# Kernel optimization log

Measured on AMD Instinct MI355X. Metric: run time of the kernel, lower is better.

Reference implementation:

```python
import jax, jax.numpy as jnp
import numpy as np

N = 50000      # nodes
E = 800000     # edges
D = 128        # d_model
H = 8          # heads
DH = D // H    # head dim
FF = 512       # dim_ff
NB = 32        # degree buckets
EPS = 1e-5


def _ln(x, g, b):
    mu = jnp.mean(x, axis=-1, keepdims=True)
    var = jnp.mean((x - mu) ** 2, axis=-1, keepdims=True)
    return (x - mu) * jax.lax.rsqrt(var + EPS) * g + b


def setup_inputs() -> dict:
    key = jax.random.key(0)
    ks = jax.random.split(key, 12)
    s = 0.02
    return {
        'x': jax.random.normal(ks[0], (N, D), jnp.float32),
        'row': jnp.sort(jax.random.randint(ks[1], (E,), 0, N, jnp.int32)),
        'col': jax.random.randint(ks[2], (E,), 0, N, jnp.int32),
        'deg_bucket': jax.random.randint(ks[3], (N,), 0, NB, jnp.int32),
        'Wq': jax.random.normal(ks[4], (D, D), jnp.float32) * s,
        'bq': jnp.zeros((D,), jnp.float32),
        'Wk': jax.random.normal(ks[5], (D, D), jnp.float32) * s,
        'bk': jnp.zeros((D,), jnp.float32),
        'Wv': jax.random.normal(ks[6], (D, D), jnp.float32) * s,
        'bv': jnp.zeros((D,), jnp.float32),
        'Wo': jax.random.normal(ks[7], (D, D), jnp.float32) * s,
        'bo': jnp.zeros((D,), jnp.float32),
        'emb': jax.random.normal(ks[8], (NB, H), jnp.float32) * s,
        'ln1_g': jnp.ones((D,), jnp.float32), 'ln1_b': jnp.zeros((D,), jnp.float32),
        'ln2_g': jnp.ones((D,), jnp.float32), 'ln2_b': jnp.zeros((D,), jnp.float32),
        'W1': jax.random.normal(ks[9], (D, FF), jnp.float32) * s,
        'b1': jnp.zeros((FF,), jnp.float32),
        'W2': jax.random.normal(ks[10], (FF, D), jnp.float32) * s,
        'b2': jnp.zeros((D,), jnp.float32),
    }


def reference(x, row, col, deg_bucket, Wq, bq, Wk, bk, Wv, bv, Wo, bo, emb,
              ln1_g, ln1_b, ln2_g, ln2_b, W1, b1, W2, b2):
    scale = DH ** (-0.5)
    Q = (x @ Wq + bq).reshape(N, H, DH)
    K = (x @ Wk + bk).reshape(N, H, DH)
    V = (x @ Wv + bv).reshape(N, H, DH)
    # edge-wise QK dot products: [E, H]
    scores = jnp.einsum('ehd,ehd->eh', Q[row], K[col]) * scale
    scores = scores + emb[deg_bucket[row]] + emb[deg_bucket[col]]
    # segment softmax over destination node `row`
    max_s = jax.ops.segment_max(scores, row, num_segments=N, indices_are_sorted=True)
    exp_s = jnp.exp(scores - max_s[row])
    sum_s = jax.ops.segment_sum(exp_s, row, num_segments=N, indices_are_sorted=True)
    alpha = exp_s / jnp.maximum(sum_s[row], 1e-12)
    # scatter-weighted aggregation of V[col]: [N, H, DH]
    agg = jax.ops.segment_sum(alpha[..., None] * V[col], row, num_segments=N,
                              indices_are_sorted=True)
    out = agg.reshape(N, D) @ Wo + bo
    h = _ln(x + out, ln1_g, ln1_b)
    ffo = jax.nn.gelu(h @ W1 + b1, approximate=False) @ W2 + b2
    return _ln(h + ffo, ln2_g, ln2_b)
```

## Files before the change

kernel.cpp:

```cpp
#include <hip/hip_runtime.h>
#include <math.h>

#define NN 50000
#define NE 800000
#define DM 128
#define NH 8
#define FF 512
#define NBLK 391
#define NBLK64 782

#define PB_X    6250
#define PB_WT   192
#define PB_RP   196
#define PB_EMB  1563
#define PB_TOT  (PB_X + PB_WT + PB_RP + PB_EMB)

typedef __attribute__((ext_vector_type(8))) short bf16x8;
typedef __attribute__((ext_vector_type(4))) float f32x4;

__device__ __forceinline__ short f2bf(float f) {
    union { float f; unsigned u; } v; v.f = f;
    unsigned r = v.u + 0x7fff + ((v.u >> 16) & 1);
    return (short)(r >> 16);
}
__device__ __forceinline__ float bf2f(short s) {
    union { unsigned u; float f; } v; v.u = ((unsigned)(unsigned short)s) << 16;
    return v.f;
}
__device__ __forceinline__ float u2f(unsigned u) {
    union { unsigned u; float f; } v; v.u = u; return v.f;
}

__device__ __forceinline__ void gload16(const void* g, void* l) {
    __builtin_amdgcn_global_load_lds(
        (const __attribute__((address_space(1))) void*)g,
        (__attribute__((address_space(3))) void*)l, 16, 0, 0);
}

__device__ __forceinline__ void stage_tile(const short* __restrict__ src, int row0,
                                           int maxrow, int ld, int col0,
                                           short* sm) {
    const int tid = threadIdx.x;
    const int w = tid >> 6, l = tid & 63;
    const int p = l & 15;
    #pragma unroll
    for (int j = 0; j < 8; ++j) {
        int lr = w * 32 + j * 4 + (l >> 4);
        int gr = row0 + lr; gr = gr > maxrow ? maxrow : gr;
        int s = p ^ (lr & 7);
        const short* g = src + (size_t)gr * ld + col0 + s * 8;
        gload16(g, sm + (w * 32 + j * 4) * 128);
    }
}

__device__ __forceinline__ void stage_tile64(const short* __restrict__ src, int row0,
                                             int maxrow, int ld, int col0,
                                             short* sm) {
    const int tid = threadIdx.x;
    const int w = tid >> 6, l = tid & 63;
    const int p = l & 15;
    #pragma unroll
    for (int j = 0; j < 4; ++j) {
        int lr = w * 16 + j * 4 + (l >> 4);
        int gr = row0 + lr; gr = gr > maxrow ? maxrow : gr;
        int s = p ^ (lr & 7);
        const short* g = src + (size_t)gr * ld + col0 + s * 8;
        gload16(g, sm + (w * 16 + j * 4) * 128);
    }
}

__device__ __forceinline__ bf16x8 frag_ld(const short* sm, int outer, int slot) {
    return *(const bf16x8*)(sm + outer * 128 + ((slot ^ (outer & 7)) << 3));
}

__device__ __forceinline__ void mfma_tile(const short* sA, const short* sB,
                                          int wm, int wn, int lane,
                                          f32x4 acc[4][4]) {
    const int l15 = lane & 15, l4 = lane >> 4;
    #pragma unroll
    for (int ks = 0; ks < 4; ++ks) {
        bf16x8 a[4], b[4];
        int slot = ks * 4 + l4;
        #pragma unroll
        for (int f = 0; f < 4; ++f) a[f] = frag_ld(sA, wm * 64 + f * 16 + l15, slot);
        #pragma unroll
        for (int f = 0; f < 4; ++f) b[f] = frag_ld(sB, wn * 64 + f * 16 + l15, slot);
        #pragma unroll
        for (int fm = 0; fm < 4; ++fm)
            #pragma unroll
            for (int fn = 0; fn < 4; ++fn)
                acc[fm][fn] = __builtin_amdgcn_mfma_f32_16x16x32_bf16(
                    a[fm], b[fn], acc[fm][fn], 0, 0, 0);
    }
}

__device__ __forceinline__ void mfma_tile64(const short* sA, const short* sB,
                                            int wm, int wn, int lane,
                                            f32x4 acc[2][4]) {
    const int l15 = lane & 15, l4 = lane >> 4;
    #pragma unroll
    for (int ks = 0; ks < 4; ++ks) {
        bf16x8 a[2], b[4];
        int slot = ks * 4 + l4;
        #pragma unroll
        for (int f = 0; f < 2; ++f) a[f] = frag_ld(sA, wm * 32 + f * 16 + l15, slot);
        #pragma unroll
        for (int f = 0; f < 4; ++f) b[f] = frag_ld(sB, wn * 64 + f * 16 + l15, slot);
        #pragma unroll
        for (int fm = 0; fm < 2; ++fm)
            #pragma unroll
            for (int fn = 0; fn < 4; ++fn)
                acc[fm][fn] = __builtin_amdgcn_mfma_f32_16x16x32_bf16(
                    a[fm], b[fn], acc[fm][fn], 0, 0, 0);
    }
}

__global__ __launch_bounds__(256) void k_prep(
    const float* __restrict__ x, short* __restrict__ xb,
    const float* __restrict__ Wq, const float* __restrict__ Wk,
    const float* __restrict__ Wv, const float* __restrict__ Wo,
    const float* __restrict__ W1, const float* __restrict__ W2,
    short* __restrict__ wts,
    const int* __restrict__ row, int* __restrict__ rowptr,
    const int* __restrict__ db, const float* __restrict__ emb,
    float* __restrict__ embn)
{
    int bid = blockIdx.x;
    const int tid = threadIdx.x;

    if (bid < PB_X) {
        int i = bid * 256 + tid;
        if (i < NN * DM / 4) {
            float4 v = ((const float4*)x)[i];
            ((short4*)xb)[i] = make_short4(f2bf(v.x), f2bf(v.y), f2bf(v.z), f2bf(v.w));
        }
        return;
    }
    bid -= PB_X;
    if (bid < PB_WT) {
        const float* W; short* Wt; int K, N, bx, by;
        if (bid < 64) {
            int wsel = bid >> 4, rel = bid & 15;
            W = wsel == 0 ? Wq : wsel == 1 ? Wk : wsel == 2 ? Wv : Wo;
            Wt = wts + wsel * 16384; K = 128; N = 128; bx = rel & 3; by = rel >> 2;
        } else if (bid < 128) {
            int rel = bid - 64;
            W = W1; Wt = wts + 65536; K = 128; N = 512; bx = rel & 15; by = rel >> 4;
        } else {
            int rel = bid - 128;
            W = W2; Wt = wts + 131072; K = 512; N = 128; bx = rel & 3; by = rel >> 2;
        }
        __shared__ float t[32][33];
        int n0 = bx * 32, k0 = by * 32;
        int r = tid >> 3, c4 = (tid & 7) * 4;
        float4 v = *(const float4*)(W + (size_t)(k0 + r) * N + n0 + c4);
        t[r][c4 + 0] = v.x; t[r][c4 + 1] = v.y; t[r][c4 + 2] = v.z; t[r][c4 + 3] = v.w;
        __syncthreads();
        short4 o = make_short4(f2bf(t[c4 + 0][r]), f2bf(t[c4 + 1][r]),
                               f2bf(t[c4 + 2][r]), f2bf(t[c4 + 3][r]));
        *(short4*)(Wt + (size_t)(n0 + r) * K + k0 + c4) = o;
        return;
    }
    bid -= PB_WT;
    if (bid < PB_RP) {
        int n = bid * 256 + tid;
        if (n > NN) return;
        int lo = 0, hi = NE;
        while (lo < hi) {
            int mid = (lo + hi) >> 1;
            if (row[mid] < n) lo = mid + 1; else hi = mid;
        }
        rowptr[n] = lo;
        return;
    }
    bid -= PB_RP;
    {
        int i = bid * 256 + tid;
        if (i < NN * NH) embn[i] = emb[db[i >> 3] * NH + (i & 7)];
    }
}

__global__ __launch_bounds__(256) void k_gemm_qkv(
    const short* __restrict__ xb, const short* __restrict__ Wt,
    const float* __restrict__ bq, const float* __restrict__ bk,
    const float* __restrict__ bv,
    short* __restrict__ Qb, short* __restrict__ Kb, short* __restrict__ Vb)
{
    __shared__ short sm[2 * 16384];
    const int tid = threadIdx.x, lane = tid & 63, wid = tid >> 6;
    const int wm = wid >> 1, wn = wid & 1;
    const int r0 = blockIdx.x * 128;

    stage_tile(xb, r0, NN - 1, 128, 0, sm);
    #pragma unroll
    for (int m = 0; m < 3; ++m) {
        if (m) __syncthreads();
        stage_tile(Wt + m * 16384, 0, 127, 128, 0, sm + 16384);
        __syncthreads();
        f32x4 acc[4][4];
        #pragma unroll
        for (int i = 0; i < 4; ++i)
            #pragma unroll
            for (int j = 0; j < 4; ++j)
                acc[i][j] = (f32x4){0.f, 0.f, 0.f, 0.f};
        mfma_tile(sm, sm + 16384, wm, wn, lane, acc);

        const float* bias = m == 0 ? bq : (m == 1 ? bk : bv);
        short* out = m == 0 ? Qb : (m == 1 ? Kb : Vb);
        #pragma unroll
        for (int fn = 0; fn < 4; ++fn) {
            int col = wn * 64 + fn * 16 + (lane & 15);
            float bc = bias[col];
            #pragma unroll
            for (int fm = 0; fm < 4; ++fm) {
                int rowb = r0 + wm * 64 + fm * 16 + (lane >> 4) * 4;
                #pragma unroll
                for (int rr = 0; rr < 4; ++rr) {
                    int gr = rowb + rr;
                    if (gr < NN)
                        out[(size_t)gr * DM + col] = f2bf(acc[fm][fn][rr] + bc);
                }
            }
        }
    }
}

__global__ __launch_bounds__(256) void k_attn_wave(
    const short* __restrict__ Qb, const short* __restrict__ Kb,
    const short* __restrict__ Vb, const int* __restrict__ col,
    const int* __restrict__ rowptr, const float* __restrict__ embn,
    short* __restrict__ aggb)
{
    const int lane = threadIdx.x & 63;
    const int n = blockIdx.x * 4 + (threadIdx.x >> 6);
    const int e0 = rowptr[n], e1 = rowptr[n + 1];
    const int s = lane >> 3, h = lane & 7;
    const int h2 = lane >> 3;

    float qf[16];
    {
        const bf16x8* qp = (const bf16x8*)(Qb + (size_t)n * DM + h * 16);
        bf16x8 q0 = qp[0], q1 = qp[1];
        #pragma unroll
        for (int j = 0; j < 8; ++j) { qf[j] = bf2f(q0[j]); qf[8 + j] = bf2f(q1[j]); }
    }
    const float embr = embn[(size_t)n * NH + h];

    float m = -INFINITY, l = 0.f, acc0 = 0.f, acc1 = 0.f;

    for (int c0 = e0; c0 < e1; c0 += 16) {
        int ea = c0 + s, eb = c0 + 8 + s;
        bool va = ea < e1, vb = eb < e1;
        int ca = col[va ? ea : e1 - 1];
        int cb = col[vb ? eb : e1 - 1];

        const bf16x8* kpa = (const bf16x8*)(Kb + (size_t)ca * DM + h * 16);
        const bf16x8* kpb = (const bf16x8*)(Kb + (size_t)cb * DM + h * 16);
        bf16x8 ka0 = kpa[0], ka1 = kpa[1];
        bf16x8 kb0 = kpb[0], kb1 = kpb[1];
        float ema = embn[(size_t)ca * NH + h];
        float emB = embn[(size_t)cb * NH + h];

        int nv = e1 - c0; nv = nv > 16 ? 16 : nv;
        unsigned vv[16];
        #pragma unroll
        for (int j = 0; j < 8; ++j) {
            int cj = __shfl(ca, j * 8);
            vv[j] = (j < nv) ? *(const unsigned*)(Vb + (size_t)cj * DM + lane * 2) : 0u;
        }
        #pragma unroll
        for (int j = 0; j < 8; ++j) {
            int cj = __shfl(cb, j * 8);
            vv[8 + j] = (8 + j < nv) ? *(const unsigned*)(Vb + (size_t)cj * DM + lane * 2) : 0u;
        }

        float da = 0.f, dbv = 0.f;
        #pragma unroll
        for (int j = 0; j < 8; ++j) {
            da  += qf[j] * bf2f(ka0[j]) + qf[8 + j] * bf2f(ka1[j]);
            dbv += qf[j] * bf2f(kb0[j]) + qf[8 + j] * bf2f(kb1[j]);
        }
        float sa = va ? da * 0.25f + embr + ema : -INFINITY;
        float sb = vb ? dbv * 0.25f + embr + emB : -INFINITY;

        float mc = fmaxf(sa, sb);
        mc = fmaxf(mc, __shfl_xor(mc, 8));
        mc = fmaxf(mc, __shfl_xor(mc, 16));
        mc = fmaxf(mc, __shfl_xor(mc, 32));
        float mn = fmaxf(m, mc);
        float f = __expf(m - mn);
        m = mn;
        float pa = __expf(sa - mn);
        float pb = __expf(sb - mn);
        float ps = pa + pb;
        ps += __shfl_xor(ps, 8);
        ps += __shfl_xor(ps, 16);
        ps += __shfl_xor(ps, 32);
        l = l * f + ps;

        float fr = __shfl(f, h2);
        acc0 *= fr; acc1 *= fr;
        #pragma unroll
        for (int j = 0; j < 8; ++j) {
            float pj = __shfl(pa, j * 8 + h2);
            acc0 += pj * u2f(vv[j] << 16);
            acc1 += pj * u2f(vv[j] & 0xffff0000u);
        }
        #pragma unroll
        for (int j = 0; j < 8; ++j) {
            float pj = __shfl(pb, j * 8 + h2);
            acc0 += pj * u2f(vv[8 + j] << 16);
            acc1 += pj * u2f(vv[8 + j] & 0xffff0000u);
        }
    }
    float la = __shfl(l, h2);
    la = fmaxf(la, 1e-12f);
    unsigned o = ((unsigned)(unsigned short)f2bf(acc0 / la)) |
                 (((unsigned)(unsigned short)f2bf(acc1 / la)) << 16);
    *(unsigned*)(aggb + (size_t)n * DM + lane * 2) = o;
}

__global__ __launch_bounds__(256) void k_gemm_ln1(
    const short* __restrict__ aggb, const short* __restrict__ Wot,
    const float* __restrict__ bo, const float* __restrict__ x,
    const float* __restrict__ g, const float* __restrict__ b,
    float* __restrict__ h, short* __restrict__ hb)
{
    __shared__ union { short ab[2 * 16384]; float hs[128 * 129]; } u;
    __shared__ float mu[128], rsd[128];
    const int tid = threadIdx.x, lane = tid & 63, wid = tid >> 6;
    const int wm = wid >> 1, wn = wid & 1;
    const int r0 = blockIdx.x * 128;

    stage_tile(aggb, r0, NN - 1, 128, 0, u.ab);
    stage_tile(Wot, 0, 127, 128, 0, u.ab + 16384);
    __syncthreads();

    f32x4 acc[4][4];
    #pragma unroll
    for (int i = 0; i < 4; ++i)
        #pragma unroll
        for (int j = 0; j < 4; ++j) acc[i][j] = (f32x4){0.f, 0.f, 0.f, 0.f};
    mfma_tile(u.ab, u.ab + 16384, wm, wn, lane, acc);
    __syncthreads();

    #pragma unroll
    for (int fn = 0; fn < 4; ++fn) {
        int col = wn * 64 + fn * 16 + (lane & 15);
        float bc = bo[col];
        #pragma unroll
        for (int fm = 0; fm < 4; ++fm) {
            int rowb = wm * 64 + fm * 16 + (lane >> 4) * 4;
            #pragma unroll
            for (int rr = 0; rr < 4; ++rr) {
                int r_ = rowb + rr, gr = r0 + r_;
                float xr = (gr < NN) ? x[(size_t)gr * DM + col] : 0.f;
                u.hs[r_ * 129 + col] = acc[fm][fn][rr] + bc + xr;
            }
        }
    }
    __syncthreads();

    {
        int rrow = tid >> 1, half = tid & 1;
        float s = 0.f, q = 0.f;
        #pragma unroll 8
        for (int c = 0; c < 64; ++c) {
            float v = u.hs[rrow * 129 + half * 64 + c];
            s += v; q += v * v;
        }
        s += __shfl_xor(s, 1);
        q += __shfl_xor(q, 1);
        float m = s * (1.f / DM);
        float var = q * (1.f / DM) - m * m;
        if (half == 0) { mu[rrow] = m; rsd[rrow] = rsqrtf(var + 1e-5f); }
    }
    __syncthreads();

    for (int i = 0; i < 64; ++i) {
        int idx = i * 256 + tid;
        int rrow = idx >> 7, c = idx & 127;
        int gr = r0 + rrow;
        if (gr < NN) {
            float v = (u.hs[rrow * 129 + c] - mu[rrow]) * rsd[rrow] * g[c] + b[c];
            h[(size_t)gr * DM + c] = v;
            hb[(size_t)gr * DM + c] = f2bf(v);
        }
    }
}

__global__ __launch_bounds__(256) void k_ffn_fused(
    const short* __restrict__ hb, const short* __restrict__ Wt1,
    const float* __restrict__ b1, const short* __restrict__ Wt2,
    const float* __restrict__ b2, const float* __restrict__ h,
    const float* __restrict__ g, const float* __restrict__ bb,
    float* __restrict__ out)
{
    extern __shared__ char smraw[];
    short* A = (short*)smraw;
    short* B = A + 8192;
    short* C = B + 16384;
    float* hs = (float*)smraw;
    __shared__ float mu[64], rsd[64];

    const int tid = threadIdx.x, lane = tid & 63, wid = tid >> 6;
    const int wm = wid >> 1, wn = wid & 1;
    const int r0 = blockIdx.x * 64;

    f32x4 acc2[2][4];
    #pragma unroll
    for (int i = 0; i < 2; ++i)
        #pragma unroll
        for (int j = 0; j < 4; ++j) acc2[i][j] = (f32x4){0.f, 0.f, 0.f, 0.f};

    stage_tile64(hb, r0, NN - 1, 128, 0, A);

    for (int kc = 0; kc < 4; ++kc) {
        if (kc) __syncthreads();
        stage_tile(Wt1, kc * 128, FF - 1, 128, 0, B);
        __syncthreads();

        f32x4 accf[2][4];
        #pragma unroll
        for (int i = 0; i < 2; ++i)
            #pragma unroll
            for (int j = 0; j < 4; ++j) accf[i][j] = (f32x4){0.f, 0.f, 0.f, 0.f};
        mfma_tile64(A, B, wm, wn, lane, accf);

        #pragma unroll
        for (int fn = 0; fn < 4; ++fn) {
            int nloc = wn * 64 + fn * 16 + (lane & 15);
            float bc = b1[kc * 128 + nloc];
            int slot = nloc >> 3;
            #pragma unroll
            for (int fm = 0; fm < 2; ++fm) {
                int rowb = wm * 32 + fm * 16 + (lane >> 4) * 4;
                #pragma unroll
                for (int rr = 0; rr < 4; ++rr) {
                    int row = rowb + rr;
                    float v = accf[fm][fn][rr] + bc;
                    v = 0.5f * v * (1.f + erff(v * 0.70710678118654752f));
                    C[row * 128 + (((slot ^ (row & 7)) << 3) | (nloc & 7))] = f2bf(v);
                }
            }
        }
        __syncthreads();
        stage_tile(Wt2, 0, 127, FF, kc * 128, B);
        __syncthreads();
        mfma_tile64(C, B, wm, wn, lane, acc2);
    }
    __syncthreads();

    #pragma unroll
    for (int fn = 0; fn < 4; ++fn) {
        int col = wn * 64 + fn * 16 + (lane & 15);
        float bc = b2[col];
        #pragma unroll
        for (int fm = 0; fm < 2; ++fm) {
            int rowb = wm * 32 + fm * 16 + (lane >> 4) * 4;
            #pragma unroll
            for (int rr = 0; rr < 4; ++rr) {
                int r_ = rowb + rr, gr = r0 + r_;
                float hr = (gr < NN) ? h[(size_t)gr * DM + col] : 0.f;
                hs[r_ * 129 + col] = acc2[fm][fn][rr] + bc + hr;
            }
        }
    }
    __syncthreads();

    {
        int rrow = tid >> 2, q = tid & 3;
        float s = 0.f, qq = 0.f;
        #pragma unroll 8
        for (int c = 0; c < 32; ++c) {
            float v = hs[rrow * 129 + q * 32 + c];
            s += v; qq += v * v;
        }
        s += __shfl_xor(s, 1);  qq += __shfl_xor(qq, 1);
        s += __shfl_xor(s, 2);  qq += __shfl_xor(qq, 2);
        float m = s * (1.f / DM);
        float var = qq * (1.f / DM) - m * m;
        if (q == 0) { mu[rrow] = m; rsd[rrow] = rsqrtf(var + 1e-5f); }
    }
    __syncthreads();

    for (int i = 0; i < 32; ++i) {
        int idx = i * 256 + tid;
        int rrow = idx >> 7, c = idx & 127;
        int gr = r0 + rrow;
        if (gr < NN)
            out[(size_t)gr * DM + c] =
                (hs[rrow * 129 + c] - mu[rrow]) * rsd[rrow] * g[c] + bb[c];
    }
}

extern "C" void kernel_launch(void* const* d_in, const int* in_sizes, int n_in,
                              void* d_out, int out_size, void* d_ws, size_t ws_size,
                              hipStream_t stream) {
    const float* x   = (const float*)d_in[0];
    const int* row   = (const int*)d_in[1];
    const int* col   = (const int*)d_in[2];
    const int* db    = (const int*)d_in[3];
    const float* Wq  = (const float*)d_in[4];
    const float* bq  = (const float*)d_in[5];
    const float* Wk  = (const float*)d_in[6];
    const float* bk  = (const float*)d_in[7];
    const float* Wv  = (const float*)d_in[8];
    const float* bv  = (const float*)d_in[9];
    const float* Wo  = (const float*)d_in[10];
    const float* bo  = (const float*)d_in[11];
    const float* emb = (const float*)d_in[12];
    const float* g1  = (const float*)d_in[13];
    const float* b1n = (const float*)d_in[14];
    const float* g2  = (const float*)d_in[15];
    const float* b2n = (const float*)d_in[16];
    const float* W1  = (const float*)d_in[17];
    const float* b1  = (const float*)d_in[18];
    const float* W2  = (const float*)d_in[19];
    const float* b2  = (const float*)d_in[20];

    char* W = (char*)d_ws;
    float* embn   = (float*)(W + 0);
    short* aggb   = (short*)(W + 25600000);
    short* xb     = (short*)(W + 38400000);
    short* Qb     = (short*)(W + 51200000);
    short* Kb     = (short*)(W + 64000000);
    float* h      = (float*)(W + 51200000);
    short* Vb     = (short*)(W + 76800000);
    short* hb     = (short*)(W + 76800000);
    short* wts    = (short*)(W + 89600000);
    int* rowptr   = (int*)(W + 89993216);

    k_prep<<<PB_TOT, 256, 0, stream>>>(x, xb, Wq, Wk, Wv, Wo, W1, W2, wts,
                                       row, rowptr, db, emb, embn);
    k_gemm_qkv<<<NBLK, 256, 0, stream>>>(xb, wts, bq, bk, bv, Qb, Kb, Vb);
    k_attn_wave<<<NN / 4, 256, 0, stream>>>(Qb, Kb, Vb, col, rowptr, embn, aggb);
    k_gemm_ln1<<<NBLK, 256, 0, stream>>>(aggb, wts + 49152, bo, x, g1, b1n, h, hb);
    k_ffn_fused<<<NBLK64, 256, 65536, stream>>>(hb, wts + 65536, b1,
                                                wts + 131072, b2, h, g2, b2n,
                                                (float*)d_out);
}
```

Before: 221.6 us.

## Store K and V in FP8 and use tanh-approximated GELU

The QKV GEMM now writes K and V as FP8 bytes instead of bf16. The attention kernel gathers half as many bytes per edge for K and V and unpacks them with the hardware FP8-to-f32 conversion. The FFN GELU switches from erf to a tanh approximation built on exp. Both changes aim to cut gather bandwidth and ALU cost. They trade away numerical accuracy, since FP8 K/V and approximate GELU may drift from the reference.

```diff
diff --git a/kernel.cpp b/kernel.cpp
--- a/kernel.cpp
+++ b/kernel.cpp
@@ -17,6 +17,7 @@
 
 typedef __attribute__((ext_vector_type(8))) short bf16x8;
 typedef __attribute__((ext_vector_type(4))) float f32x4;
+typedef __attribute__((ext_vector_type(2))) float f32x2;
 
 __device__ __forceinline__ short f2bf(float f) {
     union { float f; unsigned u; } v; v.f = f;
@@ -27,8 +28,15 @@
     union { unsigned u; float f; } v; v.u = ((unsigned)(unsigned short)s) << 16;
     return v.f;
 }
-__device__ __forceinline__ float u2f(unsigned u) {
-    union { unsigned u; float f; } v; v.u = u; return v.f;
+__device__ __forceinline__ unsigned char f2fp8(float f) {
+    int p = __builtin_amdgcn_cvt_pk_fp8_f32(f, f, 0, false);
+    return (unsigned char)(p & 0xff);
+}
+
+__device__ __forceinline__ float gelu_f(float x) {
+    float u = x * (0.7978845608f + 0.0356774081f * x * x);
+    float t = 1.f - 2.f / (__expf(2.f * u) + 1.f);
+    return 0.5f * x * (1.f + t);
 }
 
 __device__ __forceinline__ void gload16(const void* g, void* l) {
@@ -184,7 +192,8 @@
     const short* __restrict__ xb, const short* __restrict__ Wt,
     const float* __restrict__ bq, const float* __restrict__ bk,
     const float* __restrict__ bv,
-    short* __restrict__ Qb, short* __restrict__ Kb, short* __restrict__ Vb)
+    short* __restrict__ Qb, unsigned char* __restrict__ Kf8,
+    unsigned char* __restrict__ Vf8)
 {
     __shared__ short sm[2 * 16384];
     const int tid = threadIdx.x, lane = tid & 63, wid = tid >> 6;
@@ -206,7 +215,6 @@
         mfma_tile(sm, sm + 16384, wm, wn, lane, acc);
 
         const float* bias = m == 0 ? bq : (m == 1 ? bk : bv);
-        short* out = m == 0 ? Qb : (m == 1 ? Kb : Vb);
         #pragma unroll
         for (int fn = 0; fn < 4; ++fn) {
             int col = wn * 64 + fn * 16 + (lane & 15);
@@ -217,8 +225,15 @@
                 #pragma unroll
                 for (int rr = 0; rr < 4; ++rr) {
                     int gr = rowb + rr;
-                    if (gr < NN)
-                        out[(size_t)gr * DM + col] = f2bf(acc[fm][fn][rr] + bc);
+                    if (gr < NN) {
+                        float v = acc[fm][fn][rr] + bc;
+                        if (m == 0)
+                            Qb[(size_t)gr * DM + col] = f2bf(v);
+                        else if (m == 1)
+                            Kf8[(size_t)gr * DM + col] = f2fp8(v);
+                        else
+                            Vf8[(size_t)gr * DM + col] = f2fp8(v);
+                    }
                 }
             }
         }
@@ -226,8 +241,8 @@
 }
 
 __global__ __launch_bounds__(256) void k_attn_wave(
-    const short* __restrict__ Qb, const short* __restrict__ Kb,
-    const short* __restrict__ Vb, const int* __restrict__ col,
+    const short* __restrict__ Qb, const unsigned char* __restrict__ Kf8,
+    const unsigned char* __restrict__ Vf8, const int* __restrict__ col,
     const int* __restrict__ rowptr, const float* __restrict__ embn,
     short* __restrict__ aggb)
 {
@@ -254,31 +269,39 @@
         int ca = col[va ? ea : e1 - 1];
         int cb = col[vb ? eb : e1 - 1];
 
-        const bf16x8* kpa = (const bf16x8*)(Kb + (size_t)ca * DM + h * 16);
-        const bf16x8* kpb = (const bf16x8*)(Kb + (size_t)cb * DM + h * 16);
-        bf16x8 ka0 = kpa[0], ka1 = kpa[1];
-        bf16x8 kb0 = kpb[0], kb1 = kpb[1];
+        int4 kwa = *(const int4*)(Kf8 + (size_t)ca * DM + h * 16);
+        int4 kwb = *(const int4*)(Kf8 + (size_t)cb * DM + h * 16);
         float ema = embn[(size_t)ca * NH + h];
         float emB = embn[(size_t)cb * NH + h];
 
         int nv = e1 - c0; nv = nv > 16 ? 16 : nv;
-        unsigned vv[16];
+        unsigned short vv[16];
         #pragma unroll
         for (int j = 0; j < 8; ++j) {
             int cj = __shfl(ca, j * 8);
-            vv[j] = (j < nv) ? *(const unsigned*)(Vb + (size_t)cj * DM + lane * 2) : 0u;
+            vv[j] = (j < nv) ? *(const unsigned short*)(Vf8 + (size_t)cj * DM + lane * 2) : 0;
         }
         #pragma unroll
         for (int j = 0; j < 8; ++j) {
             int cj = __shfl(cb, j * 8);
-            vv[8 + j] = (8 + j < nv) ? *(const unsigned*)(Vb + (size_t)cj * DM + lane * 2) : 0u;
+            vv[8 + j] = (8 + j < nv) ? *(const unsigned short*)(Vf8 + (size_t)cj * DM + lane * 2) : 0;
         }
 
         float da = 0.f, dbv = 0.f;
-        #pragma unroll
-        for (int j = 0; j < 8; ++j) {
-            da  += qf[j] * bf2f(ka0[j]) + qf[8 + j] * bf2f(ka1[j]);
-            dbv += qf[j] * bf2f(kb0[j]) + qf[8 + j] * bf2f(kb1[j]);
+        {
+            int ka[4] = {kwa.x, kwa.y, kwa.z, kwa.w};
+            int kb[4] = {kwb.x, kwb.y, kwb.z, kwb.w};
+            #pragma unroll
+            for (int w = 0; w < 4; ++w) {
+                f32x2 alo = __builtin_amdgcn_cvt_pk_f32_fp8(ka[w], false);
+                f32x2 ahi = __builtin_amdgcn_cvt_pk_f32_fp8(ka[w], true);
+                f32x2 blo = __builtin_amdgcn_cvt_pk_f32_fp8(kb[w], false);
+                f32x2 bhi = __builtin_amdgcn_cvt_pk_f32_fp8(kb[w], true);
+                da  += qf[w * 4 + 0] * alo[0] + qf[w * 4 + 1] * alo[1]
+                     + qf[w * 4 + 2] * ahi[0] + qf[w * 4 + 3] * ahi[1];
+                dbv += qf[w * 4 + 0] * blo[0] + qf[w * 4 + 1] * blo[1]
+                     + qf[w * 4 + 2] * bhi[0] + qf[w * 4 + 3] * bhi[1];
+            }
         }
         float sa = va ? da * 0.25f + embr + ema : -INFINITY;
         float sb = vb ? dbv * 0.25f + embr + emB : -INFINITY;
@@ -303,14 +326,16 @@
         #pragma unroll
         for (int j = 0; j < 8; ++j) {
             float pj = __shfl(pa, j * 8 + h2);
-            acc0 += pj * u2f(vv[j] << 16);
-            acc1 += pj * u2f(vv[j] & 0xffff0000u);
+            f32x2 vd = __builtin_amdgcn_cvt_pk_f32_fp8((int)vv[j], false);
+            acc0 += pj * vd[0];
+            acc1 += pj * vd[1];
         }
         #pragma unroll
         for (int j = 0; j < 8; ++j) {
             float pj = __shfl(pb, j * 8 + h2);
-            acc0 += pj * u2f(vv[8 + j] << 16);
-            acc1 += pj * u2f(vv[8 + j] & 0xffff0000u);
+            f32x2 vd = __builtin_amdgcn_cvt_pk_f32_fp8((int)vv[8 + j], false);
+            acc0 += pj * vd[0];
+            acc1 += pj * vd[1];
         }
     }
     float la = __shfl(l, h2);
@@ -438,8 +463,7 @@
                 #pragma unroll
                 for (int rr = 0; rr < 4; ++rr) {
                     int row = rowb + rr;
-                    float v = accf[fm][fn][rr] + bc;
-                    v = 0.5f * v * (1.f + erff(v * 0.70710678118654752f));
+                    float v = gelu_f(accf[fm][fn][rr] + bc);
                     C[row * 128 + (((slot ^ (row & 7)) << 3) | (nloc & 7))] = f2bf(v);
                 }
             }
@@ -520,21 +544,21 @@
     const float* b2  = (const float*)d_in[20];
 
     char* W = (char*)d_ws;
-    float* embn   = (float*)(W + 0);
+    float* embn          = (float*)(W + 0);
+    unsigned char* Kf8   = (unsigned char*)(W + 1600000);
+    unsigned char* Vf8   = (unsigned char*)(W + 8000000);
     short* aggb   = (short*)(W + 25600000);
     short* xb     = (short*)(W + 38400000);
     short* Qb     = (short*)(W + 51200000);
-    short* Kb     = (short*)(W + 64000000);
     float* h      = (float*)(W + 51200000);
-    short* Vb     = (short*)(W + 76800000);
     short* hb     = (short*)(W + 76800000);
     short* wts    = (short*)(W + 89600000);
     int* rowptr   = (int*)(W + 89993216);
 
     k_prep<<<PB_TOT, 256, 0, stream>>>(x, xb, Wq, Wk, Wv, Wo, W1, W2, wts,
                                        row, rowptr, db, emb, embn);
-    k_gemm_qkv<<<NBLK, 256, 0, stream>>>(xb, wts, bq, bk, bv, Qb, Kb, Vb);
-    k_attn_wave<<<NN / 4, 256, 0, stream>>>(Qb, Kb, Vb, col, rowptr, embn, aggb);
+    k_gemm_qkv<<<NBLK, 256, 0, stream>>>(xb, wts, bq, bk, bv, Qb, Kf8, Vf8);
+    k_attn_wave<<<NN / 4, 256, 0, stream>>>(Qb, Kf8, Vf8, col, rowptr, embn, aggb);
     k_gemm_ln1<<<NBLK, 256, 0, stream>>>(aggb, wts + 49152, bo, x, g1, b1n, h, hb);
     k_ffn_fused<<<NBLK64, 256, 65536, stream>>>(hb, wts + 65536, b1,
                                                 wts + 131072, b2, h, g2, b2n,
```

Result: faster. 208.5 us (-5.9%).
